# Optimization experiments

Hardware: AMD Instinct MI355X
Metric: run time of the kernel (lower is better)

## Reference

```python
import jax, jax.numpy as jnp
import numpy as np

S_LEN = 8        # stride_length
LEVELS = 4       # corr_levels
RADIUS = 3       # corr_radius
CD = 2 * RADIUS + 1  # corr_dim = 7
PLANES = ((0, 1), (0, 2), (1, 2))  # itertools.combinations(range(3), 2)


def _bilinear(img, pts):
    # img: (C,H,W); pts: (...,2) normalized [-1,1], x->W, y->H; align_corners=True, border padding
    C, H, W = img.shape
    x = jnp.clip((pts[..., 0] + 1.0) * 0.5 * (W - 1), 0.0, W - 1.0)
    y = jnp.clip((pts[..., 1] + 1.0) * 0.5 * (H - 1), 0.0, H - 1.0)
    x0f = jnp.floor(x); y0f = jnp.floor(y)
    x0 = x0f.astype(jnp.int32); y0 = y0f.astype(jnp.int32)
    x1 = jnp.minimum(x0 + 1, W - 1); y1 = jnp.minimum(y0 + 1, H - 1)
    wx = x - x0f; wy = y - y0f
    return (img[:, y0, x0] * (1 - wy) * (1 - wx) + img[:, y0, x1] * (1 - wy) * wx
            + img[:, y1, x0] * wy * (1 - wx) + img[:, y1, x1] * wy * wx)


def _trilinear(vol, pts):
    # vol: (C,D,H,W); pts: (...,3) normalized, x->W, y->H, z->D; align_corners=True, border padding
    C, D, H, W = vol.shape
    x = jnp.clip((pts[..., 0] + 1.0) * 0.5 * (W - 1), 0.0, W - 1.0)
    y = jnp.clip((pts[..., 1] + 1.0) * 0.5 * (H - 1), 0.0, H - 1.0)
    z = jnp.clip((pts[..., 2] + 1.0) * 0.5 * (D - 1), 0.0, float(max(D - 1, 0)))
    x0f = jnp.floor(x); y0f = jnp.floor(y); z0f = jnp.floor(z)
    x0 = x0f.astype(jnp.int32); y0 = y0f.astype(jnp.int32); z0 = z0f.astype(jnp.int32)
    x1 = jnp.minimum(x0 + 1, W - 1); y1 = jnp.minimum(y0 + 1, H - 1); z1 = jnp.minimum(z0 + 1, D - 1)
    wx = x - x0f; wy = y - y0f; wz = z - z0f
    out = (vol[:, z0, y0, x0] * (1 - wz) * (1 - wy) * (1 - wx)
           + vol[:, z0, y0, x1] * (1 - wz) * (1 - wy) * wx
           + vol[:, z0, y1, x0] * (1 - wz) * wy * (1 - wx)
           + vol[:, z0, y1, x1] * (1 - wz) * wy * wx
           + vol[:, z1, y0, x0] * wz * (1 - wy) * (1 - wx)
           + vol[:, z1, y0, x1] * wz * (1 - wy) * wx
           + vol[:, z1, y1, x0] * wz * wy * (1 - wx)
           + vol[:, z1, y1, x1] * wz * wy * wx)
    return out


def setup_inputs():
    key = jax.random.key(0)
    ks = jax.random.split(key, 5)
    B, N, V, DLAT = 1, 256, 96, 128
    coords = jax.random.uniform(ks[0], (B, S_LEN, N, 3), jnp.float32) * (V - 1)
    coords_init = jax.random.uniform(ks[1], (B, N, 3), jnp.float32) * (V - 1)
    feature_planes = jax.random.normal(ks[2], (B * S_LEN, DLAT * 3, V, V), jnp.float32)
    w1 = jax.random.normal(ks[3], (CD ** 4, 384), jnp.float32) * 0.02
    b1 = jnp.zeros((384,), jnp.float32)
    w2 = jax.random.normal(ks[4], (384, 256), jnp.float32) * 0.05
    b2 = jnp.zeros((256,), jnp.float32)
    return dict(coords=coords, coords_init=coords_init, feature_planes=feature_planes,
                w1=w1, b1=b1, w2=w2, b2=b2)


def _forward(coords, coords_init, feature_planes, w1, b1, w2, b2):
    B, S, N, _ = coords.shape
    dt = coords.dtype
    off = jnp.arange(CD, dtype=dt) - RADIUS
    oc = jnp.stack(jnp.meshgrid(off, off, indexing='ij'), -1)        # (7,7,2) spatial offsets
    oc3 = jnp.concatenate([oc, jnp.zeros_like(oc[..., :1])], -1)     # (7,7,3) zero time offset
    # ---- init_levels: feature pyramid + initial track features ----
    fp = feature_planes  # ((B S), (D*3), V, V)
    fplevels, tflevels = [], []
    for i in range(LEVELS):
        if i > 0:
            bs, c, v, _ = fp.shape
            fp = fp.reshape(bs, c, v // 2, 2, v // 2, 2).mean(axis=(3, 5))  # avg_pool2d(2,2)
        bs, c, v, _ = fp.shape
        d = c // 3
        lev = fp.reshape(B, S, d, 3, v, v).transpose(0, 1, 2, 4, 5, 3)  # (B,S,d,v,v,planes)
        fplevels.append(lev)
        scale3 = jnp.array([v - 1, v - 1, S - 1], dt)
        # time coordinate = batch index (faithful to get_track_features t construction)
        t = jnp.broadcast_to(jnp.arange(B, dtype=dt)[:, None, None], (B, N, 1))
        tfs = []
        for k, (a, b2_) in enumerate(PLANES):
            c3 = jnp.concatenate([coords_init[..., (a, b2_)] / (2.0 ** i), t], -1)  # (B,N,3)
            reg = c3[:, None, None, :, :] + oc3[None, :, :, None, :]  # (B,7,7,N,3)
            g = reg * (2.0 / scale3) - 1.0
            vol = lev[..., k].transpose(0, 2, 1, 3, 4)  # (B,d,S,v,v)
            samp = jax.vmap(_trilinear)(vol, g)          # (B,d,7,7,N)
            tfs.append(samp.reshape(B, d, CD * CD, N).transpose(0, 2, 3, 1))  # (B,49,N,d)
        tflevels.append(jnp.stack(tfs, -1))  # (B,49,N,d,planes)
    # ---- get_corr_features: per-level 4D correlation volumes + corr_mlp ----
    outs = []
    for i in range(LEVELS):
        lev = fplevels[i]
        v = lev.shape[3]; d = lev.shape[2]
        scale2 = jnp.array([v - 1, v - 1], dt)
        acc = None
        for k, (a, b2_) in enumerate(PLANES):
            c2 = (coords[..., (a, b2_)] / (2.0 ** i)).reshape(B * S, N, 2)
            reg = c2[:, :, None, None, :] + oc[None, None, :, :, :]  # (BS,N,7,7,2)
            g = reg * (2.0 / scale2) - 1.0
            frames = lev[..., k].reshape(B * S, d, v, v)
            cf2 = jax.vmap(_bilinear)(frames, g)                     # (BS,d,N,7,7)
            cf2 = cf2.transpose(0, 2, 3, 4, 1).reshape(B, S, N, CD, CD, d)  # b s n h w d
            tf = tflevels[i][..., k].transpose(0, 2, 3, 1).reshape(B, N, d, CD, CD)  # b n d x y
            c4 = jnp.einsum('bsnhwd,bndxy->bsnhwxy', cf2, tf).reshape(B * S * N, CD ** 4)
            h = jax.nn.gelu(c4 @ w1 + b1, approximate=True)
            o = h @ w2 + b2
            acc = o if acc is None else acc + o
        outs.append(acc)
    return jnp.concatenate(outs, -1).reshape(B, S, N, LEVELS * w2.shape[1])


def reference(coords, coords_init, feature_planes, w1, b1, w2, b2):
    return _forward(coords, coords_init, feature_planes, w1, b1, w2, b2)
```

## Files before the change

### kernel.cpp

```cpp
#include <hip/hip_runtime.h>
#include <hip/hip_bf16.h>
#include <math.h>

#define NTRK 256
#define DLAT 128
#define CDIM 7
#define CD2  49
#define CD4  2401
#define NH1  384
#define NH2  256
#define LDK  2432
#define PITCHB 272
#define CPITCH 272

#define SZ_L0 ((size_t)3 * 8 * 96 * 96 * 128)
#define SZ_L1 ((size_t)3 * 8 * 48 * 48 * 128)
#define SZ_L2 ((size_t)3 * 8 * 24 * 24 * 128)
#define SZ_L3 ((size_t)3 * 8 * 12 * 12 * 128)
#define SZ_TF ((size_t)3 * NTRK * DLAT * CD2)

typedef __attribute__((ext_vector_type(8))) short short8;
typedef __attribute__((ext_vector_type(4))) float f32x4;
typedef __attribute__((ext_vector_type(4))) unsigned int u32x4;


__device__ __forceinline__ float b2f(unsigned short u) {
    union { unsigned int i; float f; } c;
    c.i = ((unsigned int)u) << 16;
    return c.f;
}
__device__ __forceinline__ unsigned int f2b(float x) {
    __hip_bfloat16 h = __float2bfloat16(x);
    return (unsigned int)(*(unsigned short*)&h);
}

__device__ __forceinline__ float gelu_tanh(float x) {
    float x2 = x * x;
    float p = x * fmaf(0.044715f, x2, 1.0f);
    float e = __expf(-1.5957691216f * p);
    return __fdividef(x, 1.0f + e);
}

__device__ __forceinline__ int plane_a(int k) { return (k == 2) ? 1 : 0; }
__device__ __forceinline__ int plane_b(int k) { return (k == 0) ? 1 : 2; }

__device__ __forceinline__ int lev_v(int lev) { return 96 >> lev; }
__device__ __forceinline__ size_t lev_off(int lev) {
    return (lev > 0 ? SZ_L0 : 0) + (lev > 1 ? SZ_L1 : 0) + (lev > 2 ? SZ_L2 : 0);
}

__device__ __forceinline__ void gload16(const void* g, void* l) {
    __builtin_amdgcn_global_load_lds(
        (const __attribute__((address_space(1))) unsigned int*)g,
        (__attribute__((address_space(3))) unsigned int*)l,
        16, 0, 0);
}


__global__ __launch_bounds__(256) void cvt_cl_kernel(const float* __restrict__ in,
                                                     __hip_bfloat16* __restrict__ out) {
    __shared__ unsigned int lds[64][97];
    const int b = blockIdx.x;
    const int y = b % 96;
    const int ks = b / 96;
    const int k = ks >> 3, s = ks & 7;
    const int tid = threadIdx.x;
    for (int idx = tid; idx < 64 * 24; idx += 256) {
        int d2 = idx / 24, x4 = (idx - d2 * 24) * 4;
        const float* rlo = in + (((size_t)s * 384 + (2 * d2) * 3 + k) * 96 + y) * 96 + x4;
        const float* rhi = in + (((size_t)s * 384 + (2 * d2 + 1) * 3 + k) * 96 + y) * 96 + x4;
        float4 lo = *(const float4*)rlo;
        float4 hi = *(const float4*)rhi;
        lds[d2][x4 + 0] = f2b(lo.x) | (f2b(hi.x) << 16);
        lds[d2][x4 + 1] = f2b(lo.y) | (f2b(hi.y) << 16);
        lds[d2][x4 + 2] = f2b(lo.z) | (f2b(hi.z) << 16);
        lds[d2][x4 + 3] = f2b(lo.w) | (f2b(hi.w) << 16);
    }
    __syncthreads();
    unsigned int* orow = (unsigned int*)((unsigned short*)out + ((size_t)ks * 96 + y) * 96 * 128);
    for (int idx = tid; idx < 96 * 16; idx += 256) {
        int x = idx >> 4, q = idx & 15;
        u32x4 r;
        r[0] = lds[4 * q + 0][x];
        r[1] = lds[4 * q + 1][x];
        r[2] = lds[4 * q + 2][x];
        r[3] = lds[4 * q + 3][x];
        *(u32x4*)(orow + x * 64 + q * 4) = r;
    }
}


__global__ __launch_bounds__(256) void pool_cl(const __hip_bfloat16* __restrict__ in,
                                               __hip_bfloat16* __restrict__ out,
                                               int vin, int total8) {
    int idx = blockIdx.x * 256 + threadIdx.x;
    if (idx >= total8) return;
    int vout = vin >> 1;
    int d8 = idx & 15;
    int t = idx >> 4;
    int x = t % vout; t /= vout;
    int y = t % vout; t /= vout;
    const unsigned short* base = (const unsigned short*)in
        + (((size_t)t * vin + 2 * y) * vin + 2 * x) * 128 + d8 * 8;
    short8 a = *(const short8*)(base);
    short8 bq = *(const short8*)(base + 128);
    short8 c = *(const short8*)(base + (size_t)vin * 128);
    short8 d = *(const short8*)(base + (size_t)vin * 128 + 128);
    short8 r;
    #pragma unroll
    for (int j = 0; j < 8; ++j) {
        float sum = b2f((unsigned short)a[j]) + b2f((unsigned short)bq[j])
                  + b2f((unsigned short)c[j]) + b2f((unsigned short)d[j]);
        r[j] = (short)f2b(0.25f * sum);
    }
    *(short8*)((unsigned short*)out + ((((size_t)t * vout + y) * vout + x)) * 128 + d8 * 8) = r;
}


__global__ __launch_bounds__(256) void tf_all(const __hip_bfloat16* __restrict__ levbase,
                                              const float* __restrict__ coords_init,
                                              __hip_bfloat16* __restrict__ tfb) {
    const int bid = blockIdx.x;
    const int lev = bid / 768;
    const int r0 = bid - lev * 768;
    const int g = (r0 & 7) * 96 + (r0 >> 3);
    const int k = g >> 8;
    const int n = g & 255;
    const int v = lev_v(lev);
    const float inv_scale = 1.f / (float)(1 << lev);
    const float vm1 = (float)(v - 1);
    float cx = coords_init[n * 3 + plane_a(k)] * inv_scale;
    float cy = coords_init[n * 3 + plane_b(k)] * inv_scale;
    const unsigned short* frame = (const unsigned short*)levbase + lev_off(lev)
        + (size_t)(k * 8) * v * v * 128;
    unsigned short* dst = (unsigned short*)tfb + (size_t)lev * SZ_TF
        + ((size_t)(k * NTRK + n)) * (DLAT * CD2);
    for (int idx = threadIdx.x; idx < CD2 * 16; idx += 256) {
        int xy = idx >> 4;
        int c8 = idx & 15;
        int i = xy / CDIM, j = xy % CDIM;
        float X = fminf(fmaxf(cx + (float)(i - 3), 0.f), vm1);
        float Y = fminf(fmaxf(cy + (float)(j - 3), 0.f), vm1);
        float xf = floorf(X), yf = floorf(Y);
        int x0 = (int)xf, y0 = (int)yf;
        int x1 = min(x0 + 1, v - 1), y1 = min(y0 + 1, v - 1);
        float wx = X - xf, wy = Y - yf;
        const unsigned short* r00 = frame + ((size_t)y0 * v + x0) * 128 + c8 * 8;
        const unsigned short* r01 = frame + ((size_t)y0 * v + x1) * 128 + c8 * 8;
        const unsigned short* r10 = frame + ((size_t)y1 * v + x0) * 128 + c8 * 8;
        const unsigned short* r11 = frame + ((size_t)y1 * v + x1) * 128 + c8 * 8;
        short8 a = *(const short8*)r00, bq = *(const short8*)r01;
        short8 c = *(const short8*)r10, d = *(const short8*)r11;
        float w00 = (1.f - wy) * (1.f - wx), w01 = (1.f - wy) * wx;
        float w10 = wy * (1.f - wx), w11 = wy * wx;
        short8 r;
        #pragma unroll
        for (int e = 0; e < 8; ++e) {
            float val = b2f((unsigned short)a[e]) * w00 + b2f((unsigned short)bq[e]) * w01
                      + b2f((unsigned short)c[e]) * w10 + b2f((unsigned short)d[e]) * w11;
            r[e] = (short)f2b(val);
        }
        *(short8*)(dst + xy * 128 + c8 * 8) = r;
    }
}


__global__ __launch_bounds__(256) void corr_all(const __hip_bfloat16* __restrict__ levbase,
                                                const float* __restrict__ coords,
                                                const __hip_bfloat16* __restrict__ tfb,
                                                __hip_bfloat16* __restrict__ c4b) {
    __shared__ __align__(16) char patch[64 * PITCHB];
    __shared__ __align__(16) char tfs[64 * PITCHB];
    __shared__ __align__(16) char cbuf[64 * CPITCH];
    __shared__ float wxs[2][8], wys[2][8];
    const int bid = blockIdx.x;
    const int lk = bid >> 8;
    const int n = bid & 255;
    const int lev = lk / 3;
    const int k = lk - lev * 3;
    const int v = lev_v(lev);
    const int vv = v * v;
    const float inv_scale = 1.f / (float)(1 << lev);
    const int tid = threadIdx.x;
    const float vm1 = (float)(v - 1);

    const short8* tfg = (const short8*)(tfb + (size_t)lev * SZ_TF
        + ((size_t)(k * NTRK + n)) * (DLAT * CD2));
    for (int idx = tid; idx < 784; idx += 256) {
        int row = idx >> 4, c16 = idx & 15;
        *(short8*)(tfs + row * PITCHB + c16 * 16) = tfg[idx];
    }

    const int hwb = tid / 49;
    const int xy  = tid - hwb * 49;
    const bool act = tid < 245;

    const unsigned short* fbase = (const unsigned short*)levbase + lev_off(lev)
        + (size_t)(k * 8) * vv * 128;
    const int w4 = tid >> 6, l = tid & 63;
    const int l15 = l & 15, l4 = l >> 4;

    const int c8 = tid & 15;
    const int posb = tid >> 4;

    float cxc, cyc; int fxc, fyc;
    short8 pre[4];

    auto CALC = [&](int s) {
        const int sn = s * 256 + n;
        cxc = coords[sn * 3 + plane_a(k)] * inv_scale;
        cyc = coords[sn * 3 + plane_b(k)] * inv_scale;
        fxc = (int)floorf(cxc);
        fyc = (int)floorf(cyc);
    };
    auto PREF = [&](int s) {
        const unsigned short* frame = fbase + (size_t)s * vv * 128;
        #pragma unroll
        for (int q = 0; q < 4; ++q) {
            int pos = posb + 16 * q;
            int px = pos & 7, py = pos >> 3;
            int gx = min(max(fxc + px - 3, 0), v - 1);
            int gy = min(max(fyc + py - 3, 0), v - 1);
            pre[q] = *(const short8*)(frame + ((size_t)gy * v + gx) * 128 + c8 * 8);
        }
    };
    auto INTERP = [&](int sp) {
        unsigned short* crow = (unsigned short*)c4b + ((size_t)lk * 2048 + sp * 256 + n) * LDK;
        const int p = sp & 1;
        if (act) {
            int h = 0, w = hwb;
            unsigned short* op = crow + tid;
            const char* colbase = cbuf + xy * 4;
            #pragma unroll
            for (int it = 0; it < 10; ++it) {
                if (h < 7) {
                    float wxv = wxs[p][h], wyv = wys[p][w];
                    const char* tap = colbase + (w * 8 + h) * CPITCH;
                    float p00 = *(const float*)(tap);
                    float p01 = *(const float*)(tap + CPITCH);
                    float p10 = *(const float*)(tap + 8 * CPITCH);
                    float p11 = *(const float*)(tap + 9 * CPITCH);
                    float a  = fmaf(wxv, p01 - p00, p00);
                    float bq = fmaf(wxv, p11 - p10, p10);
                    *op = (unsigned short)f2b(fmaf(wyv, bq - a, a));
                }
                w += 5; if (w >= 7) { w -= 7; h += 1; }
                op += 245;
            }
        }
        if (tid < LDK - CD4) crow[CD4 + tid] = 0;
    };

    CALC(0); PREF(0);
    for (int s = 0; s < 8; ++s) {
        #pragma unroll
        for (int q = 0; q < 4; ++q)
            *(short8*)(patch + (posb + 16 * q) * PITCHB + c8 * 16) = pre[q];
        if (tid < 7) {
            float X = fminf(fmaxf(cxc + (float)(tid - 3), 0.f), vm1);
            int g = min(max(fxc + tid - 3, 0), v - 1);
            wxs[s & 1][tid] = X - (float)g;
            float Y = fminf(fmaxf(cyc + (float)(tid - 3), 0.f), vm1);
            int gy_ = min(max(fyc + tid - 3, 0), v - 1);
            wys[s & 1][tid] = Y - (float)gy_;
        }
        if (s > 0) INTERP(s - 1);
        __syncthreads();

        f32x4 acc[4];
        #pragma unroll
        for (int nt = 0; nt < 4; ++nt) acc[nt] = (f32x4){0.f, 0.f, 0.f, 0.f};
        #pragma unroll
        for (int ks = 0; ks < 4; ++ks) {
            short8 af = *(const short8*)(patch + (16 * w4 + l15) * PITCHB + ks * 64 + l4 * 16);
            #pragma unroll
            for (int nt = 0; nt < 4; ++nt) {
                short8 bf = *(const short8*)(tfs + (16 * nt + l15) * PITCHB + ks * 64 + l4 * 16);
                acc[nt] = __builtin_amdgcn_mfma_f32_16x16x32_bf16(af, bf, acc[nt], 0, 0, 0);
            }
        }
        if (s < 7) { CALC(s + 1); PREF(s + 1); }
        {
            const int row0 = 16 * w4 + l4 * 4;
            #pragma unroll
            for (int nt = 0; nt < 4; ++nt) {
                int col = nt * 16 + l15;
                #pragma unroll
                for (int j = 0; j < 4; ++j)
                    *(float*)(cbuf + (row0 + j) * CPITCH + col * 4) = acc[nt][j];
            }
        }
        __syncthreads();
    }
    INTERP(7);
}


__global__ __launch_bounds__(256) void prep_w1t(const float* __restrict__ w1,
                                                __hip_bfloat16* __restrict__ w1t) {
    __shared__ float t[64][65];
    const int kk0 = blockIdx.x * 64, n0 = blockIdx.y * 64;
    const int tid = threadIdx.x;
    for (int idx = tid; idx < 4096; idx += 256) {
        int r = idx >> 6, c = idx & 63;
        int kk = kk0 + r;
        t[r][c] = (kk < CD4) ? w1[(size_t)kk * NH1 + n0 + c] : 0.f;
    }
    __syncthreads();
    for (int idx = tid; idx < 4096; idx += 256) {
        int r = idx >> 6, c = idx & 63;
        w1t[(size_t)(n0 + r) * LDK + kk0 + c] = __float2bfloat16(t[c][r]);
    }
}

__global__ __launch_bounds__(256) void prep_w2t(const float* __restrict__ w2,
                                                __hip_bfloat16* __restrict__ w2t) {
    int idx = blockIdx.x * 256 + threadIdx.x;
    if (idx >= NH2 * NH1) return;
    int n = idx / NH1, j = idx - n * NH1;
    w2t[idx] = __float2bfloat16(w2[(size_t)j * NH2 + n]);
}


__global__ __launch_bounds__(256) void gemm1_all(
    const __hip_bfloat16* __restrict__ A,
    const __hip_bfloat16* __restrict__ Bt,
    const float* __restrict__ b1,
    __hip_bfloat16* __restrict__ H) {
    __shared__ __align__(16) char smem[16384];
    char* Asm = smem;
    char* Bsm = smem + 8192;
    const int m0 = blockIdx.x * 128, n0 = blockIdx.y * 128;
    const int tid = threadIdx.x;
    const int w = tid >> 6, l = tid & 63;
    const int wr = w >> 1, wc = w & 1;
    const int l15 = l & 15, l4 = l >> 4;
    f32x4 acc[4][4];
    #pragma unroll
    for (int m = 0; m < 4; ++m)
        #pragma unroll
        for (int n = 0; n < 4; ++n) acc[m][n] = (f32x4){0.f, 0.f, 0.f, 0.f};
    const char* Ag = (const char*)(A + (size_t)(m0 + (tid >> 2)) * LDK) + (tid & 3) * 16;
    const char* Bg = (const char*)(Bt + (size_t)(n0 + (tid >> 2)) * LDK) + (tid & 3) * 16;
    char* AsmW = Asm + w * 1024;
    char* BsmW = Bsm + w * 1024;
    for (int kb = 0; kb < LDK * 2; kb += 64) {
        gload16(Ag + kb, AsmW);
        gload16(Ag + (size_t)64 * LDK * 2 + kb, AsmW + 4096);
        gload16(Bg + kb, BsmW);
        gload16(Bg + (size_t)64 * LDK * 2 + kb, BsmW + 4096);
        __syncthreads();
        short8 af[4], bfr[4];
        #pragma unroll
        for (int m = 0; m < 4; ++m)
            af[m] = *(const short8*)(Asm + (wr * 64 + m * 16 + l15) * 64 + l4 * 16);
        #pragma unroll
        for (int n = 0; n < 4; ++n)
            bfr[n] = *(const short8*)(Bsm + (wc * 64 + n * 16 + l15) * 64 + l4 * 16);
        #pragma unroll
        for (int m = 0; m < 4; ++m)
            #pragma unroll
            for (int n = 0; n < 4; ++n)
                acc[m][n] = __builtin_amdgcn_mfma_f32_16x16x32_bf16(af[m], bfr[n], acc[m][n], 0, 0, 0);
        __syncthreads();
    }
    #pragma unroll
    for (int m = 0; m < 4; ++m) {
        int row = m0 + wr * 64 + m * 16 + l4 * 4;
        #pragma unroll
        for (int n = 0; n < 4; ++n) {
            int col = n0 + wc * 64 + n * 16 + l15;
            float bias = b1[col];
            #pragma unroll
            for (int j = 0; j < 4; ++j)
                H[(size_t)(row + j) * NH1 + col] = __float2bfloat16(gelu_tanh(acc[m][n][j] + bias));
        }
    }
}


__global__ __launch_bounds__(256) void gemm2_all(
    const __hip_bfloat16* __restrict__ Hin,
    const __hip_bfloat16* __restrict__ Bt,
    const float* __restrict__ b2,
    float* __restrict__ out) {
    __shared__ __align__(16) char smem[8192];
    char* Asm = smem;
    char* Bsm = smem + 4096;
    const int lev = blockIdx.x >> 5;
    const int m0 = (blockIdx.x & 31) * 64, n0 = blockIdx.y * 64;
    const int tid = threadIdx.x;
    const int w = tid >> 6, l = tid & 63;
    const int wr = w >> 1, wc = w & 1;
    const int l15 = l & 15, l4 = l >> 4;
    f32x4 acc[2][2];
    #pragma unroll
    for (int m = 0; m < 2; ++m)
        #pragma unroll
        for (int n = 0; n < 2; ++n) acc[m][n] = (f32x4){0.f, 0.f, 0.f, 0.f};
    const char* Bg = (const char*)(Bt + (size_t)(n0 + (tid >> 2)) * NH1) + (tid & 3) * 16;
    char* AsmW = Asm + w * 1024;
    char* BsmW = Bsm + w * 1024;
    for (int p = 0; p < 3; ++p) {
        const char* Ag = (const char*)(Hin
            + (size_t)((lev * 3 + p) * 2048 + m0 + (tid >> 2)) * NH1) + (tid & 3) * 16;
        for (int jb = 0; jb < NH1 * 2; jb += 64) {
            gload16(Ag + jb, AsmW);
            gload16(Bg + jb, BsmW);
            __syncthreads();
            short8 af[2], bfr[2];
            #pragma unroll
            for (int m = 0; m < 2; ++m)
                af[m] = *(const short8*)(Asm + (wr * 32 + m * 16 + l15) * 64 + l4 * 16);
            #pragma unroll
            for (int n = 0; n < 2; ++n)
                bfr[n] = *(const short8*)(Bsm + (wc * 32 + n * 16 + l15) * 64 + l4 * 16);
            #pragma unroll
            for (int m = 0; m < 2; ++m)
                #pragma unroll
                for (int n = 0; n < 2; ++n)
                    acc[m][n] = __builtin_amdgcn_mfma_f32_16x16x32_bf16(af[m], bfr[n], acc[m][n], 0, 0, 0);
            __syncthreads();
        }
    }
    #pragma unroll
    for (int m = 0; m < 2; ++m) {
        int row = m0 + wr * 32 + m * 16 + l4 * 4;
        #pragma unroll
        for (int n = 0; n < 2; ++n) {
            int col = n0 + wc * 32 + n * 16 + l15;
            float bias3 = 3.f * b2[col];
            #pragma unroll
            for (int j = 0; j < 4; ++j)
                out[(size_t)(row + j) * 1024 + lev * NH2 + col] = acc[m][n][j] + bias3;
        }
    }
}


extern "C" void kernel_launch(void* const* d_in, const int* in_sizes, int n_in,
                              void* d_out, int out_size, void* d_ws, size_t ws_size,
                              hipStream_t stream) {
    const float* coords      = (const float*)d_in[0];
    const float* coords_init = (const float*)d_in[1];
    const float* fp0         = (const float*)d_in[2];
    const float* w1          = (const float*)d_in[3];
    const float* b1          = (const float*)d_in[4];
    const float* w2          = (const float*)d_in[5];
    const float* b2          = (const float*)d_in[6];
    float* out = (float*)d_out;
    char* ws = (char*)d_ws;

    __hip_bfloat16* lev0 = (__hip_bfloat16*)ws;      ws += SZ_L0 * 2;
    __hip_bfloat16* lev1 = (__hip_bfloat16*)ws;      ws += SZ_L1 * 2;
    __hip_bfloat16* lev2 = (__hip_bfloat16*)ws;      ws += SZ_L2 * 2;
    __hip_bfloat16* lev3 = (__hip_bfloat16*)ws;      ws += SZ_L3 * 2;
    __hip_bfloat16* tfb  = (__hip_bfloat16*)ws;      ws += (size_t)4 * SZ_TF * 2;
    __hip_bfloat16* c4b  = (__hip_bfloat16*)ws;      ws += (size_t)24576 * LDK * 2;
    __hip_bfloat16* h_ws = (__hip_bfloat16*)ws;      ws += (size_t)24576 * NH1 * 2;
    __hip_bfloat16* w1t  = (__hip_bfloat16*)ws;      ws += (size_t)NH1 * LDK * 2;
    __hip_bfloat16* w2t  = (__hip_bfloat16*)ws;      ws += (size_t)NH2 * NH1 * 2;

    prep_w1t<<<dim3(38, 6), 256, 0, stream>>>(w1, w1t);
    prep_w2t<<<(NH2 * NH1 + 255) / 256, 256, 0, stream>>>(w2, w2t);

    cvt_cl_kernel<<<24 * 96, 256, 0, stream>>>(fp0, lev0);
    pool_cl<<<(int)((SZ_L1 / 8 + 255) / 256), 256, 0, stream>>>(lev0, lev1, 96, (int)(SZ_L1 / 8));
    pool_cl<<<(int)((SZ_L2 / 8 + 255) / 256), 256, 0, stream>>>(lev1, lev2, 48, (int)(SZ_L2 / 8));
    pool_cl<<<(int)((SZ_L3 / 8 + 255) / 256), 256, 0, stream>>>(lev2, lev3, 24, (int)(SZ_L3 / 8));

    tf_all<<<4 * 768, 256, 0, stream>>>(lev0, coords_init, tfb);
    corr_all<<<3072, 256, 0, stream>>>(lev0, coords, tfb, c4b);
    gemm1_all<<<dim3(192, 3), 256, 0, stream>>>(c4b, w1t, b1, h_ws);
    gemm2_all<<<dim3(128, 4), 256, 0, stream>>>(h_ws, w2t, b2, out);
}
```

Measured before the change: 262.0 us.

## Keep corr B fragments in registers, reuse LDS, and swizzle gemm1 block order

```diff
diff --git a/kernel.cpp b/kernel.cpp
--- a/kernel.cpp
+++ b/kernel.cpp
@@ -11,7 +11,6 @@
 #define NH2  256
 #define LDK  2432
 #define PITCHB 272
-#define CPITCH 272
 
 #define SZ_L0 ((size_t)3 * 8 * 96 * 96 * 128)
 #define SZ_L1 ((size_t)3 * 8 * 48 * 48 * 128)
@@ -165,13 +164,12 @@
 }
 
 
-__global__ __launch_bounds__(256) void corr_all(const __hip_bfloat16* __restrict__ levbase,
-                                                const float* __restrict__ coords,
-                                                const __hip_bfloat16* __restrict__ tfb,
-                                                __hip_bfloat16* __restrict__ c4b) {
+__global__ __launch_bounds__(256, 4) void corr_all(const __hip_bfloat16* __restrict__ levbase,
+                                                   const float* __restrict__ coords,
+                                                   const __hip_bfloat16* __restrict__ tfb,
+                                                   __hip_bfloat16* __restrict__ c4b) {
     __shared__ __align__(16) char patch[64 * PITCHB];
-    __shared__ __align__(16) char tfs[64 * PITCHB];
-    __shared__ __align__(16) char cbuf[64 * CPITCH];
+    __shared__ __align__(16) char cbuf[64 * PITCHB];
     __shared__ float wxs[2][8], wys[2][8];
     const int bid = blockIdx.x;
     const int lk = bid >> 8;
@@ -184,12 +182,23 @@
     const int tid = threadIdx.x;
     const float vm1 = (float)(v - 1);
 
+    const int w4 = tid >> 6, l = tid & 63;
+    const int l15 = l & 15, l4 = l >> 4;
+
     const short8* tfg = (const short8*)(tfb + (size_t)lev * SZ_TF
         + ((size_t)(k * NTRK + n)) * (DLAT * CD2));
     for (int idx = tid; idx < 784; idx += 256) {
         int row = idx >> 4, c16 = idx & 15;
-        *(short8*)(tfs + row * PITCHB + c16 * 16) = tfg[idx];
-    }
+        *(short8*)(cbuf + row * PITCHB + c16 * 16) = tfg[idx];
+    }
+    __syncthreads();
+
+    short8 bfr[4][4];
+    #pragma unroll
+    for (int nt = 0; nt < 4; ++nt)
+        #pragma unroll
+        for (int ks = 0; ks < 4; ++ks)
+            bfr[nt][ks] = *(const short8*)(cbuf + (16 * nt + l15) * PITCHB + ks * 64 + l4 * 16);
 
     const int hwb = tid / 49;
     const int xy  = tid - hwb * 49;
@@ -197,8 +206,6 @@
 
     const unsigned short* fbase = (const unsigned short*)levbase + lev_off(lev)
         + (size_t)(k * 8) * vv * 128;
-    const int w4 = tid >> 6, l = tid & 63;
-    const int l15 = l & 15, l4 = l >> 4;
 
     const int c8 = tid & 15;
     const int posb = tid >> 4;
@@ -235,11 +242,11 @@
             for (int it = 0; it < 10; ++it) {
                 if (h < 7) {
                     float wxv = wxs[p][h], wyv = wys[p][w];
-                    const char* tap = colbase + (w * 8 + h) * CPITCH;
+                    const char* tap = colbase + (w * 8 + h) * PITCHB;
                     float p00 = *(const float*)(tap);
-                    float p01 = *(const float*)(tap + CPITCH);
-                    float p10 = *(const float*)(tap + 8 * CPITCH);
-                    float p11 = *(const float*)(tap + 9 * CPITCH);
+                    float p01 = *(const float*)(tap + PITCHB);
+                    float p10 = *(const float*)(tap + 8 * PITCHB);
+                    float p11 = *(const float*)(tap + 9 * PITCHB);
                     float a  = fmaf(wxv, p01 - p00, p00);
                     float bq = fmaf(wxv, p11 - p10, p10);
                     *op = (unsigned short)f2b(fmaf(wyv, bq - a, a));
@@ -274,10 +281,8 @@
         for (int ks = 0; ks < 4; ++ks) {
             short8 af = *(const short8*)(patch + (16 * w4 + l15) * PITCHB + ks * 64 + l4 * 16);
             #pragma unroll
-            for (int nt = 0; nt < 4; ++nt) {
-                short8 bf = *(const short8*)(tfs + (16 * nt + l15) * PITCHB + ks * 64 + l4 * 16);
-                acc[nt] = __builtin_amdgcn_mfma_f32_16x16x32_bf16(af, bf, acc[nt], 0, 0, 0);
-            }
+            for (int nt = 0; nt < 4; ++nt)
+                acc[nt] = __builtin_amdgcn_mfma_f32_16x16x32_bf16(af, bfr[nt][ks], acc[nt], 0, 0, 0);
         }
         if (s < 7) { CALC(s + 1); PREF(s + 1); }
         {
@@ -287,7 +292,7 @@
                 int col = nt * 16 + l15;
                 #pragma unroll
                 for (int j = 0; j < 4; ++j)
-                    *(float*)(cbuf + (row0 + j) * CPITCH + col * 4) = acc[nt][j];
+                    *(float*)(cbuf + (row0 + j) * PITCHB + col * 4) = acc[nt][j];
             }
         }
         __syncthreads();
@@ -330,7 +335,10 @@
     __shared__ __align__(16) char smem[16384];
     char* Asm = smem;
     char* Bsm = smem + 8192;
-    const int m0 = blockIdx.x * 128, n0 = blockIdx.y * 128;
+    const int id = blockIdx.x;
+    const int gq = id / 24, rq = id - gq * 24;
+    const int m0 = (gq * 8 + (rq & 7)) * 128;
+    const int n0 = (rq >> 3) * 128;
     const int tid = threadIdx.x;
     const int w = tid >> 6, l = tid & 63;
     const int wr = w >> 1, wc = w & 1;
@@ -471,6 +479,6 @@
 
     tf_all<<<4 * 768, 256, 0, stream>>>(lev0, coords_init, tfb);
     corr_all<<<3072, 256, 0, stream>>>(lev0, coords, tfb, c4b);
-    gemm1_all<<<dim3(192, 3), 256, 0, stream>>>(c4b, w1t, b1, h_ws);
+    gemm1_all<<<576, 256, 0, stream>>>(c4b, w1t, b1, h_ws);
     gemm2_all<<<dim3(128, 4), 256, 0, stream>>>(h_ws, w2t, b2, out);
 }
```

Result: slower. 434.6 us (+65.9%).
